# Performance work log

Measured on AMD Instinct MI355X. Metric: run time of the kernel, lower is better.

Reference implementation:

```python
import jax, jax.numpy as jnp
import numpy as np

B, L, D_IN = 16, 2048, 512
HID, H = 512, 8
D = HID // H          # head dim
FACTOR = 5
U = min(FACTOR * int(np.ceil(np.log(L))), L)  # u_q == u_k == 40 (L == S)


def setup_inputs() -> dict:
    key = jax.random.key(0)
    ks = jax.random.split(key, 8)
    s = 1.0 / np.sqrt(D_IN).astype(np.float32)
    return {
        "q_in": jax.random.normal(ks[0], (B, L, D_IN), jnp.float32),
        "k_in": jax.random.normal(ks[1], (B, L, D_IN), jnp.float32),
        "v_in": jax.random.normal(ks[2], (B, L, D_IN), jnp.float32),
        "Wq": jax.random.normal(ks[3], (D_IN, HID), jnp.float32) * s,
        "Wk": jax.random.normal(ks[4], (D_IN, HID), jnp.float32) * s,
        "Wv": jax.random.normal(ks[5], (D_IN, HID), jnp.float32) * s,
        "Wo": jax.random.normal(ks[6], (HID, HID // H), jnp.float32) / np.sqrt(HID).astype(np.float32),
        "indx_q_seq": jax.random.randint(ks[7], (L,), 0, L, dtype=jnp.int32),
    }


def reference(q_in, k_in, v_in, Wq, Wk, Wv, Wo, indx_q_seq):
    # projections + (memory-reinterpreting, as in the TF source) head reshape
    q = (q_in @ Wq).reshape(B, H, L, D)
    k = (k_in @ Wk).reshape(B, H, L, D)
    v = (v_in @ Wv).reshape(B, H, L, D)

    # --- _prob_qk ---
    # TF's chained gathers on the broadcast k_expand collapse to pairing
    # query s with the single key indx_q_seq[s]; all sample_k columns of
    # Q_K_sample are identical, so M = max - sum/L = dot * (1 - U/L).
    k_sel = k[:, :, indx_q_seq, :]                        # [B,H,L,D]
    dot = jnp.einsum('bhle,bhle->bhl', q, k_sel)          # [B,H,L]
    M = dot - dot * (jnp.float32(U) / jnp.float32(L))
    _, m_top = jax.lax.top_k(M, U)                        # [B,H,U]

    b_idx = jnp.arange(B)[:, None, None]
    h_idx = jnp.arange(H)[None, :, None]
    q_red = q[b_idx, h_idx, m_top]                        # [B,H,U,D]
    scores = jnp.einsum('bhue,bhle->bhul', q_red, k)      # [B,H,U,L]
    scores = scores * (1.0 / np.sqrt(D).astype(np.float32))

    # --- initial context: causal cumsum of values ---
    context = jnp.cumsum(v, axis=-2)                      # [B,H,L,D]

    # --- update context at the top-U query positions (causal mask) ---
    causal = jnp.arange(L)[None, None, None, :] > m_top[..., None]
    scores = jnp.where(causal, -jnp.inf, scores)
    attn = jax.nn.softmax(scores, axis=-1)                # [B,H,U,L]
    upd = jnp.einsum('bhul,bhld->bhud', attn, v)          # [B,H,U,D]
    context = context.at[b_idx, h_idx, m_top].set(upd)

    out = context.reshape(B, L, HID) @ Wo                 # [B,L,HID//H]
    return out
```

## Files before the change

### kernel.cpp

```cpp
#include <hip/hip_runtime.h>
#include <hip/hip_bf16.h>
#include <math.h>

#define B_   16
#define L_   2048
#define DIN  512
#define HID_ 512
#define H_   8
#define D_   64
#define U_   40
#define BH   (B_*H_)

typedef unsigned short u16;
typedef unsigned int u32;
typedef unsigned long long u64;
typedef __bf16 bf16x8 __attribute__((ext_vector_type(8)));
typedef float f32x4 __attribute__((ext_vector_type(4)));

__device__ __forceinline__ u16 f2bf(float x) {
  __bf16 b = (__bf16)x;
  return __builtin_bit_cast(unsigned short, b);
}
__device__ __forceinline__ float bf2f(u16 h) {
  return __uint_as_float(((unsigned)h) << 16);
}
__device__ __forceinline__ u32 pk2(float a, float b) {
  return (u32)f2bf(a) | ((u32)f2bf(b) << 16);
}
__device__ __forceinline__ void gload16(const u16* g, u16* l) {
  __builtin_amdgcn_global_load_lds(
      (__attribute__((address_space(1))) void*)(g),
      (__attribute__((address_space(3))) void*)(l), 16, 0, 0);
}
__device__ __forceinline__ void gload16f(const float* g, float* l) {
  __builtin_amdgcn_global_load_lds(
      (__attribute__((address_space(1))) void*)(g),
      (__attribute__((address_space(3))) void*)(l), 16, 0, 0);
}
__device__ __forceinline__ u64 mkkey(float Mv, int l) {
  u32 fb = __float_as_uint(Mv);
  u32 mapped = (fb & 0x80000000u) ? ~fb : (fb | 0x80000000u);
  return ((u64)mapped << 32) | (u64)(0xFFFFFFFFu - (u32)l);
}

__global__ __launch_bounds__(256)
void wsplit3_kernel(const float* __restrict__ Wq, const float* __restrict__ Wk,
                    const float* __restrict__ Wv, u16* __restrict__ Bt3) {
  const float* W = (blockIdx.y == 0) ? Wq : (blockIdx.y == 1) ? Wk : Wv;
  u16* Bt = Bt3 + (size_t)blockIdx.y * 524288;
  int tid = blockIdx.x * 256 + threadIdx.x;
  int n = tid & 511, k = tid >> 9;
  float a = W[(size_t)k * 512 + n];
  u16 hi = f2bf(a);
  u16 lo = f2bf(a - bf2f(hi));
  int kb = k >> 5, kc = k & 31;
  int slotH = kc >> 3, wi = kc & 7;
  int swzH = (slotH     ^ (n & 7)) << 3;
  int swzL = ((4+slotH) ^ (n & 7)) << 3;
  Bt[(size_t)n * 1024 + kb * 64 + swzH + wi] = hi;
  Bt[(size_t)n * 1024 + kb * 64 + swzL + wi] = lo;
}

__global__ __launch_bounds__(256, 2)
void gemm_proj3(const float* __restrict__ A, const u16* __restrict__ Bt,
                float* __restrict__ C) {
  __shared__ float Asf[2][128 * 32];
  __shared__ u16 Bs[2][128 * 64];
  const int bid = blockIdx.x;
  const int g = bid >> 3;
  const int xb = (bid & 7) + ((g >> 2) << 3);
  const int yb = g & 3;
  const int t = threadIdx.x;
  const int w = t >> 6, lane = t & 63;
  const int lhi = lane >> 4, l16 = lane & 15;
  const int row0 = xb * 128, col0 = yb * 128;
  const int wrow = (w >> 1) * 64, wcol = (w & 1) * 64;

  const u16* gB = Bt + (size_t)(col0 + w * 32 + (lane >> 3)) * 1024 + (lane & 7) * 8;
  const int rA0 = w * 32 + (lane >> 3);
  const int swsl = lane & 7;

  f32x4 acc[4][4];
  #pragma unroll
  for (int i = 0; i < 4; ++i)
    #pragma unroll
    for (int j = 0; j < 4; ++j) acc[i][j] = (f32x4){0.f, 0.f, 0.f, 0.f};

#define STAGE3(KB, NB)                                                          \
  { u16* lB = &Bs[NB][(w * 32) * 64];                                           \
    _Pragma("unroll") for (int i = 0; i < 4; ++i)                               \
      gload16(gB + (KB) * 64 + (size_t)i * 8 * 1024, lB + i * 8 * 64);          \
    _Pragma("unroll") for (int i = 0; i < 4; ++i) {                             \
      int r = rA0 + i * 8;                                                      \
      int slot = swsl ^ (r & 7);                                                \
      gload16f(A + (size_t)(row0 + r) * 512 + (KB) * 32 + slot * 4,             \
               &Asf[NB][(w * 32 + i * 8) * 32]); } }

  STAGE3(0, 0)
  asm volatile("s_waitcnt vmcnt(0)" ::: "memory");
  __builtin_amdgcn_s_barrier();

  for (int kb = 0; kb < 16; ++kb) {
    const int cur = kb & 1;
    if (kb < 15) {
      STAGE3(kb + 1, cur ^ 1)
      asm volatile("s_waitcnt vmcnt(8)" ::: "memory");
    } else {
      asm volatile("s_waitcnt vmcnt(0)" ::: "memory");
    }
    __builtin_amdgcn_sched_barrier(0);
    __builtin_amdgcn_s_barrier();

    bf16x8 bfH[4], bfL[4];
    #pragma unroll
    for (int j = 0; j < 4; ++j) {
      int cb = wcol + j * 16 + l16;
      bfH[j] = *reinterpret_cast<const bf16x8*>(
          &Bs[cur][cb * 64 + ((lhi ^ (cb & 7)) << 3)]);
      bfL[j] = *reinterpret_cast<const bf16x8*>(
          &Bs[cur][cb * 64 + (((4 + lhi) ^ (cb & 7)) << 3)]);
    }
    #pragma unroll
    for (int i = 0; i < 4; ++i) {
      int ra = wrow + i * 16 + l16;
      const f32x4 x0 = *reinterpret_cast<const f32x4*>(
          &Asf[cur][ra * 32 + (((lhi * 2)       ^ (ra & 7)) << 2)]);
      const f32x4 x1 = *reinterpret_cast<const f32x4*>(
          &Asf[cur][ra * 32 + ((((lhi * 2) + 1) ^ (ra & 7)) << 2)]);
      bf16x8 aH;
      aH[0] = (__bf16)x0[0]; aH[1] = (__bf16)x0[1];
      aH[2] = (__bf16)x0[2]; aH[3] = (__bf16)x0[3];
      aH[4] = (__bf16)x1[0]; aH[5] = (__bf16)x1[1];
      aH[6] = (__bf16)x1[2]; aH[7] = (__bf16)x1[3];
      #pragma unroll
      for (int j = 0; j < 4; ++j)
        acc[i][j] = __builtin_amdgcn_mfma_f32_16x16x32_bf16(aH, bfH[j], acc[i][j], 0, 0, 0);
      bf16x8 aL;
      aL[0] = (__bf16)(x0[0] - (float)aH[0]); aL[1] = (__bf16)(x0[1] - (float)aH[1]);
      aL[2] = (__bf16)(x0[2] - (float)aH[2]); aL[3] = (__bf16)(x0[3] - (float)aH[3]);
      aL[4] = (__bf16)(x1[0] - (float)aH[4]); aL[5] = (__bf16)(x1[1] - (float)aH[5]);
      aL[6] = (__bf16)(x1[2] - (float)aH[6]); aL[7] = (__bf16)(x1[3] - (float)aH[7]);
      #pragma unroll
      for (int j = 0; j < 4; ++j)
        acc[i][j] = __builtin_amdgcn_mfma_f32_16x16x32_bf16(aH, bfL[j], acc[i][j], 0, 0, 0);
      #pragma unroll
      for (int j = 0; j < 4; ++j)
        acc[i][j] = __builtin_amdgcn_mfma_f32_16x16x32_bf16(aL, bfH[j], acc[i][j], 0, 0, 0);
    }
    __builtin_amdgcn_s_barrier();
    __builtin_amdgcn_sched_barrier(0);
  }
#undef STAGE3
  #pragma unroll
  for (int i = 0; i < 4; ++i)
    #pragma unroll
    for (int j = 0; j < 4; ++j)
      #pragma unroll
      for (int r = 0; r < 4; ++r)
        C[(size_t)(row0 + wrow + i * 16 + lhi * 4 + r) * 512
          + col0 + wcol + j * 16 + l16] = acc[i][j][r];
}

__global__ __launch_bounds__(256, 2)
void gemm_proj_v(const float* __restrict__ A, const u16* __restrict__ Bt,
                 u16* __restrict__ C) {
  __shared__ float Asf[2][128 * 32];
  __shared__ u16 Bs[2][128 * 64];
  const int bid = blockIdx.x;
  const int g = bid >> 3;
  const int xb = (bid & 7) + ((g >> 2) << 3);
  const int yb = g & 3;
  const int t = threadIdx.x;
  const int w = t >> 6, lane = t & 63;
  const int lhi = lane >> 4, l16 = lane & 15;
  const int row0 = xb * 128, col0 = yb * 128;
  const int wrow = (w >> 1) * 64, wcol = (w & 1) * 64;

  const u16* gB = Bt + (size_t)(col0 + w * 32 + (lane >> 3)) * 1024 + (lane & 7) * 8;
  const int rA0 = w * 32 + (lane >> 3);
  const int swsl = lane & 7;

  f32x4 acc[4][4];
  #pragma unroll
  for (int i = 0; i < 4; ++i)
    #pragma unroll
    for (int j = 0; j < 4; ++j) acc[i][j] = (f32x4){0.f, 0.f, 0.f, 0.f};

#define STAGEV(KB, NB)                                                          \
  { u16* lB = &Bs[NB][(w * 32) * 64];                                           \
    _Pragma("unroll") for (int i = 0; i < 4; ++i)                               \
      gload16(gB + (KB) * 64 + (size_t)i * 8 * 1024, lB + i * 8 * 64);          \
    _Pragma("unroll") for (int i = 0; i < 4; ++i) {                             \
      int r = rA0 + i * 8;                                                      \
      int slot = swsl ^ (r & 7);                                                \
      gload16f(A + (size_t)(row0 + r) * 512 + (KB) * 32 + slot * 4,             \
               &Asf[NB][(w * 32 + i * 8) * 32]); } }

  STAGEV(0, 0)
  asm volatile("s_waitcnt vmcnt(0)" ::: "memory");
  __builtin_amdgcn_s_barrier();

  for (int kb = 0; kb < 16; ++kb) {
    const int cur = kb & 1;
    if (kb < 15) {
      STAGEV(kb + 1, cur ^ 1)
      asm volatile("s_waitcnt vmcnt(8)" ::: "memory");
    } else {
      asm volatile("s_waitcnt vmcnt(0)" ::: "memory");
    }
    __builtin_amdgcn_sched_barrier(0);
    __builtin_amdgcn_s_barrier();

    bf16x8 bfH[4];
    #pragma unroll
    for (int j = 0; j < 4; ++j) {
      int cb = wcol + j * 16 + l16;
      bfH[j] = *reinterpret_cast<const bf16x8*>(
          &Bs[cur][cb * 64 + ((lhi ^ (cb & 7)) << 3)]);
    }
    #pragma unroll
    for (int i = 0; i < 4; ++i) {
      int ra = wrow + i * 16 + l16;
      const f32x4 x0 = *reinterpret_cast<const f32x4*>(
          &Asf[cur][ra * 32 + (((lhi * 2)       ^ (ra & 7)) << 2)]);
      const f32x4 x1 = *reinterpret_cast<const f32x4*>(
          &Asf[cur][ra * 32 + ((((lhi * 2) + 1) ^ (ra & 7)) << 2)]);
      bf16x8 aH;
      aH[0] = (__bf16)x0[0]; aH[1] = (__bf16)x0[1];
      aH[2] = (__bf16)x0[2]; aH[3] = (__bf16)x0[3];
      aH[4] = (__bf16)x1[0]; aH[5] = (__bf16)x1[1];
      aH[6] = (__bf16)x1[2]; aH[7] = (__bf16)x1[3];
      #pragma unroll
      for (int j = 0; j < 4; ++j)
        acc[i][j] = __builtin_amdgcn_mfma_f32_16x16x32_bf16(aH, bfH[j], acc[i][j], 0, 0, 0);
    }
    __builtin_amdgcn_s_barrier();
    __builtin_amdgcn_sched_barrier(0);
  }
#undef STAGEV
  #pragma unroll
  for (int i = 0; i < 4; ++i)
    #pragma unroll
    for (int j = 0; j < 4; ++j)
      #pragma unroll
      for (int r = 0; r < 4; ++r)
        C[(size_t)(row0 + wrow + i * 16 + lhi * 4 + r) * 512
          + col0 + wcol + j * 16 + l16] = f2bf(acc[i][j][r]);
}

__global__ __launch_bounds__(256)
void dotsel_kernel(const float* __restrict__ qp, const float* __restrict__ kp,
                   const int* __restrict__ indx, u64* __restrict__ cand) {
  __shared__ u64 keys[256];
  __shared__ u64 wmax[2][4];
  const int bh = blockIdx.x, ch = blockIdx.y;
  const int t = threadIdx.x, w = t >> 6, lane = t & 63;
  const size_t boff = (size_t)bh * 131072;
  const int l0 = ch * 256 + w * 64;
  const float cUL = 40.0f / 2048.0f;
  const int li = lane >> 4;
  const int dq = lane & 15;

  #pragma unroll 8
  for (int i = 0; i < 16; ++i) {
    int l = l0 + i * 4 + li;
    int ls = indx[l];
    float4 q4 = *reinterpret_cast<const float4*>(&qp[boff + (size_t)l * 64 + dq * 4]);
    float4 k4 = *reinterpret_cast<const float4*>(&kp[boff + (size_t)ls * 64 + dq * 4]);
    float p = q4.x * k4.x + q4.y * k4.y + q4.z * k4.z + q4.w * k4.w;
    p += __shfl_xor(p, 1, 64);
    p += __shfl_xor(p, 2, 64);
    p += __shfl_xor(p, 4, 64);
    p += __shfl_xor(p, 8, 64);
    if (dq == 0) {
      float Mv = p - p * cUL;
      keys[w * 64 + i * 4 + li] = mkkey(Mv, l);
    }
  }
  __syncthreads();

  u64 myk = keys[t];
  for (int u = 0; u < U_; ++u) {
    u64 b = myk;
    #pragma unroll
    for (int off = 32; off >= 1; off >>= 1) {
      u64 v = __shfl_xor(b, off, 64);
      if (v > b) b = v;
    }
    if (lane == 0) wmax[u & 1][w] = b;
    __syncthreads();
    const u64* wm = wmax[u & 1];
    u64 m = wm[0];
    if (wm[1] > m) m = wm[1];
    if (wm[2] > m) m = wm[2];
    if (wm[3] > m) m = wm[3];
    if (myk == m) myk = 0;
    if (t == 0) cand[((size_t)(bh * 8 + ch)) * U_ + u] = m;
  }
}

__global__ __launch_bounds__(256)
void merge_topk_wo(const u64* __restrict__ cand, int* __restrict__ mtop,
                   const float* __restrict__ Wo, u16* __restrict__ WoT) {
  const int bh = blockIdx.x;
  const int t = threadIdx.x;
  {
    int tid = bh * 256 + t;
    int j = tid >> 9, k = tid & 511;
    float v = Wo[(size_t)k * 64 + j];
    int k0 = k & ~63, ko = k & 63;
    int ks = ko >> 5, kc = ko & 31;
    int slot = (ks * 4 + (kc >> 3)) ^ (j & 7);
    WoT[(size_t)j * 512 + k0 + (slot << 3) + (kc & 7)] = f2bf(v);
  }
  if (t >= 64) return;
  const int lane = t;
  u64 c0 = cand[(size_t)bh * 320 + 0 * 64 + lane];
  u64 c1 = cand[(size_t)bh * 320 + 1 * 64 + lane];
  u64 c2 = cand[(size_t)bh * 320 + 2 * 64 + lane];
  u64 c3 = cand[(size_t)bh * 320 + 3 * 64 + lane];
  u64 c4 = cand[(size_t)bh * 320 + 4 * 64 + lane];
  for (int u = 0; u < U_; ++u) {
    u64 b = c0;
    if (c1 > b) b = c1;
    if (c2 > b) b = c2;
    if (c3 > b) b = c3;
    if (c4 > b) b = c4;
    #pragma unroll
    for (int off = 32; off >= 1; off >>= 1) {
      u64 v = __shfl_xor(b, off, 64);
      if (v > b) b = v;
    }
    if (c0 == b) c0 = 0;
    if (c1 == b) c1 = 0;
    if (c2 == b) c2 = 0;
    if (c3 == b) c3 = 0;
    if (c4 == b) c4 = 0;
    if (lane == 0) mtop[bh * U_ + u] = (int)(0xFFFFFFFFu - (u32)b);
  }
}

__global__ __launch_bounds__(256)
void gather_q_kernel(const float* __restrict__ qp, const int* __restrict__ mtop,
                     u16* __restrict__ qredbf) {
  int tid = blockIdx.x * 256 + threadIdx.x;
  int s = tid >> 6;
  int d = tid & 63;
  int bh = s / 48;
  int u = s - bh * 48;
  float val = 0.f;
  if (u < U_) {
    int m = mtop[bh * U_ + u];
    val = qp[(size_t)bh * (L_ * D_) + (size_t)m * D_ + d] * 0.125f;
  }
  qredbf[tid] = f2bf(val);
}

__global__ __launch_bounds__(256)
void attn_fused(const u16* __restrict__ qredbf, const float* __restrict__ kp,
                const u16* __restrict__ vbf, const int* __restrict__ mtop,
                float* __restrict__ partial, float* __restrict__ msums) {
  __shared__ u16 As[48 * 64];
  __shared__ u16 Bs[128 * 64];
  __shared__ u16 Ps[48 * 128];
  __shared__ int ms[48];
  __shared__ float redm[4][48];
  __shared__ float reds[4][48];
  const int bh = blockIdx.x, chk = blockIdx.y;
  const int l0 = chk * 128;
  const int t = threadIdx.x, w = t >> 6, lane = t & 63;
  const int lhi = lane >> 4, l16 = lane & 15;

  for (int e = t; e < 384; e += 256) {
    int r = e >> 3, s = e & 7;
    *reinterpret_cast<uint4*>(&As[r * 64 + ((s ^ (r & 7)) << 3)]) =
        *reinterpret_cast<const uint4*>(&qredbf[(size_t)bh * 3072 + e * 8]);
  }
  #pragma unroll
  for (int ee = 0; ee < 4; ++ee) {
    int e = t + ee * 256;
    int r = e >> 3, s = e & 7;
    const float* src = &kp[(size_t)bh * 131072 + (size_t)(l0 + r) * 64 + s * 8];
    float4 va = *reinterpret_cast<const float4*>(src);
    float4 vb = *reinterpret_cast<const float4*>(src + 4);
    uint4 w4 = make_uint4(pk2(va.x, va.y), pk2(va.z, va.w),
                          pk2(vb.x, vb.y), pk2(vb.z, vb.w));
    *reinterpret_cast<uint4*>(&Bs[r * 64 + ((s ^ (r & 7)) << 3)]) = w4;
  }
  if (t < 48) ms[t] = (t < U_) ? mtop[bh * U_ + t] : -1;
  __syncthreads();

  f32x4 acc[3][2];
  #pragma unroll
  for (int m = 0; m < 3; ++m)
    #pragma unroll
    for (int n = 0; n < 2; ++n) acc[m][n] = (f32x4){0.f, 0.f, 0.f, 0.f};
  #pragma unroll
  for (int ks = 0; ks < 2; ++ks) {
    bf16x8 a[3], b[2];
    #pragma unroll
    for (int m = 0; m < 3; ++m) {
      int r = m * 16 + l16;
      a[m] = *reinterpret_cast<const bf16x8*>(
          &As[r * 64 + (((ks * 4 + lhi) ^ (r & 7)) << 3)]);
    }
    #pragma unroll
    for (int n = 0; n < 2; ++n) {
      int cb = w * 32 + n * 16 + l16;
      b[n] = *reinterpret_cast<const bf16x8*>(
          &Bs[cb * 64 + (((ks * 4 + lhi) ^ (cb & 7)) << 3)]);
    }
    #pragma unroll
    for (int m = 0; m < 3; ++m)
      #pragma unroll
      for (int n = 0; n < 2; ++n)
        acc[m][n] = __builtin_amdgcn_mfma_f32_16x16x32_bf16(a[m], b[n], acc[m][n], 0, 0, 0);
  }

  float val[3][2][4], mx[3][4];
  #pragma unroll
  for (int m = 0; m < 3; ++m)
    #pragma unroll
    for (int r = 0; r < 4; ++r) {
      int u = m * 16 + lhi * 4 + r;
      float v0 = acc[m][0][r], v1 = acc[m][1][r];
      if (l0 + w * 32 + 0 * 16 + l16 > ms[u]) v0 = -INFINITY;
      if (l0 + w * 32 + 1 * 16 + l16 > ms[u]) v1 = -INFINITY;
      val[m][0][r] = v0; val[m][1][r] = v1;
      mx[m][r] = fmaxf(v0, v1);
    }
  #pragma unroll
  for (int off = 1; off <= 8; off <<= 1)
    #pragma unroll
    for (int m = 0; m < 3; ++m)
      #pragma unroll
      for (int r = 0; r < 4; ++r)
        mx[m][r] = fmaxf(mx[m][r], __shfl_xor(mx[m][r], off, 64));
  if (l16 == 0) {
    #pragma unroll
    for (int m = 0; m < 3; ++m)
      #pragma unroll
      for (int r = 0; r < 4; ++r)
        redm[w][m * 16 + lhi * 4 + r] = mx[m][r];
  }
  __syncthreads();

  float sx[3][4];
  #pragma unroll
  for (int m = 0; m < 3; ++m)
    #pragma unroll
    for (int r = 0; r < 4; ++r) {
      int u = m * 16 + lhi * 4 + r;
      float mv = fmaxf(fmaxf(redm[0][u], redm[1][u]), fmaxf(redm[2][u], redm[3][u]));
      mv = (mv > -1e30f) ? mv : 0.f;
      float p0 = __expf(val[m][0][r] - mv);
      float p1 = __expf(val[m][1][r] - mv);
      sx[m][r] = p0 + p1;
      {
        int l = w * 32 + 0 * 16 + l16, s = l >> 3;
        int sw = (s & 8) | ((s & 7) ^ (u & 7));
        Ps[u * 128 + (sw << 3) + (l & 7)] = f2bf(p0);
      }
      {
        int l = w * 32 + 1 * 16 + l16, s = l >> 3;
        int sw = (s & 8) | ((s & 7) ^ (u & 7));
        Ps[u * 128 + (sw << 3) + (l & 7)] = f2bf(p1);
      }
    }
  #pragma unroll
  for (int off = 1; off <= 8; off <<= 1)
    #pragma unroll
    for (int m = 0; m < 3; ++m)
      #pragma unroll
      for (int r = 0; r < 4; ++r)
        sx[m][r] += __shfl_xor(sx[m][r], off, 64);
  if (l16 == 0) {
    #pragma unroll
    for (int m = 0; m < 3; ++m)
      #pragma unroll
      for (int r = 0; r < 4; ++r)
        reds[w][m * 16 + lhi * 4 + r] = sx[m][r];
  }
  __syncthreads();

  if (t < 48) {
    float mv = fmaxf(fmaxf(redm[0][t], redm[1][t]), fmaxf(redm[2][t], redm[3][t]));
    mv = (mv > -1e30f) ? mv : 0.f;
    float sv = reds[0][t] + reds[1][t] + reds[2][t] + reds[3][t];
    size_t o = (((size_t)chk * 128 + bh) * 48 + t) * 2;
    msums[o] = mv; msums[o + 1] = sv;
  }
  const size_t vbase = (size_t)bh * 131072;
  #pragma unroll
  for (int j = 0; j < 16; ++j) {
    int ll = w * 32 + 2 * j;
    u16 ua = vbf[vbase + (size_t)(l0 + ll) * 64 + lane];
    u16 ub = vbf[vbase + (size_t)(l0 + ll + 1) * 64 + lane];
    u32 pk = (u32)ua | ((u32)ub << 16);
    int s = ll >> 3;
    int sw = (s & 8) | ((s & 7) ^ (lane & 7));
    *reinterpret_cast<u32*>(&Bs[lane * 128 + (sw << 3) + (ll & 7)]) = pk;
  }
  __syncthreads();

  f32x4 acc2[3];
  #pragma unroll
  for (int m = 0; m < 3; ++m) acc2[m] = (f32x4){0.f, 0.f, 0.f, 0.f};
  #pragma unroll
  for (int ks = 0; ks < 4; ++ks) {
    bf16x8 b;
    { int cb = w * 16 + l16; int s = ks * 4 + lhi;
      int sw = (s & 8) | ((s & 7) ^ (cb & 7));
      b = *reinterpret_cast<const bf16x8*>(&Bs[cb * 128 + (sw << 3)]); }
    #pragma unroll
    for (int m = 0; m < 3; ++m) {
      int r = m * 16 + l16; int s = ks * 4 + lhi;
      int sw = (s & 8) | ((s & 7) ^ (r & 7));
      bf16x8 a = *reinterpret_cast<const bf16x8*>(&Ps[r * 128 + (sw << 3)]);
      acc2[m] = __builtin_amdgcn_mfma_f32_16x16x32_bf16(a, b, acc2[m], 0, 0, 0);
    }
  }
  #pragma unroll
  for (int m = 0; m < 3; ++m)
    #pragma unroll
    for (int r = 0; r < 4; ++r) {
      int u = m * 16 + lhi * 4 + r;
      partial[(((size_t)chk * 128 + bh) * 48 + u) * 64 + w * 16 + l16] = acc2[m][r];
    }
}

__global__ __launch_bounds__(256)
void cumsumA(const u16* __restrict__ vbf, float* __restrict__ seg32) {
  int bh = blockIdx.x, sg = blockIdx.y;
  int t = threadIdx.x, w = t >> 6, lane = t & 63;
  int g = sg * 4 + w;
  size_t base = (size_t)bh * 131072 + (size_t)g * 32 * 64;
  float s = 0.f;
  for (int i = 0; i < 32; ++i) s += bf2f(vbf[base + i * 64 + lane]);
  seg32[((size_t)bh * 64 + g) * 64 + lane] = s;
}
__global__ __launch_bounds__(256)
void cumsumB(const u16* __restrict__ vbf, const float* __restrict__ seg32,
             u16* __restrict__ ctxbf) {
  int bh = blockIdx.x, sg = blockIdx.y;
  int t = threadIdx.x, w = t >> 6, lane = t & 63;
  int g = sg * 4 + w;
  float run = 0.f;
  for (int s = 0; s < g; ++s) run += seg32[((size_t)bh * 64 + s) * 64 + lane];
  size_t base = (size_t)bh * 131072 + (size_t)g * 32 * 64;
  for (int i = 0; i < 32; ++i) {
    run += bf2f(vbf[base + i * 64 + lane]);
    ctxbf[base + i * 64 + lane] = f2bf(run);
  }
}

__global__ __launch_bounds__(256)
void merge_pv_scatter(const float* __restrict__ partial, const float* __restrict__ msums,
                      const int* __restrict__ mtop, u16* __restrict__ ctxbf) {
  int tid = blockIdx.x * 256 + threadIdx.x;
  int s = tid >> 6, d = tid & 63;
  int bh = s / U_, u = s - bh * U_;
  float mg = -INFINITY;
  #pragma unroll
  for (int c = 0; c < 16; ++c)
    mg = fmaxf(mg, msums[(((size_t)c * 128 + bh) * 48 + u) * 2]);
  float av = 0.f, sg = 0.f;
  #pragma unroll
  for (int c = 0; c < 16; ++c) {
    size_t o = (((size_t)c * 128 + bh) * 48 + u) * 2;
    float e = __expf(msums[o] - mg);
    av += partial[(((size_t)c * 128 + bh) * 48 + u) * 64 + d] * e;
    sg += msums[o + 1] * e;
  }
  ctxbf[(size_t)bh * 131072 + (size_t)mtop[s] * 64 + d] = f2bf(av / sg);
}

__global__ __launch_bounds__(256, 6)
void gemm_out(const u16* __restrict__ ctxbf, const u16* __restrict__ WoT,
              float* __restrict__ out) {
  __shared__ u16 As[64 * 64];
  __shared__ u16 Bs[64 * 64];
  const int t = threadIdx.x, w = t >> 6, lane = t & 63;
  const int lhi = lane >> 4, l16 = lane & 15;
  const int row0 = blockIdx.x * 64;
  f32x4 acc[4];
  #pragma unroll
  for (int j = 0; j < 4; ++j) acc[j] = (f32x4){0.f, 0.f, 0.f, 0.f};

  for (int k0 = 0; k0 < 512; k0 += 64) {
    #pragma unroll
    for (int ii = 0; ii < 2; ++ii) {
      int e = t + ii * 256;
      int j = e >> 3, s = e & 7;
      gload16(WoT + (size_t)j * 512 + k0 + s * 8, Bs + (size_t)(w * 64 + ii * 256) * 8);
    }
    #pragma unroll
    for (int ii = 0; ii < 2; ++ii) {
      int e = t + ii * 256;
      int r = e >> 3, s = e & 7;
      gload16(ctxbf + (size_t)(row0 + r) * 512 + k0 + (s ^ (r & 7)) * 8,
              As + (size_t)(w * 64 + ii * 256) * 8);
    }
    __syncthreads();
    #pragma unroll
    for (int ks = 0; ks < 2; ++ks) {
      int r = w * 16 + l16;
      bf16x8 a = *reinterpret_cast<const bf16x8*>(
          &As[r * 64 + (((ks * 4 + lhi) ^ (r & 7)) << 3)]);
      #pragma unroll
      for (int jf = 0; jf < 4; ++jf) {
        int cb = jf * 16 + l16;
        bf16x8 b = *reinterpret_cast<const bf16x8*>(
            &Bs[cb * 64 + (((ks * 4 + lhi) ^ (cb & 7)) << 3)]);
        acc[jf] = __builtin_amdgcn_mfma_f32_16x16x32_bf16(a, b, acc[jf], 0, 0, 0);
      }
    }
    __syncthreads();
  }
  #pragma unroll
  for (int jf = 0; jf < 4; ++jf)
    #pragma unroll
    for (int r = 0; r < 4; ++r)
      out[(size_t)(row0 + w * 16 + lhi * 4 + r) * 64 + jf * 16 + l16] = acc[jf][r];
}

extern "C" void kernel_launch(void* const* d_in, const int* in_sizes, int n_in,
                              void* d_out, int out_size, void* d_ws, size_t ws_size,
                              hipStream_t stream) {
  const float* q_in = (const float*)d_in[0];
  const float* k_in = (const float*)d_in[1];
  const float* v_in = (const float*)d_in[2];
  const float* Wq   = (const float*)d_in[3];
  const float* Wk   = (const float*)d_in[4];
  const float* Wv   = (const float*)d_in[5];
  const float* Wo   = (const float*)d_in[6];
  const int*   indx = (const int*)d_in[7];
  float* out = (float*)d_out;

  float* ws = (float*)d_ws;
  float* qp   = ws;
  float* kp   = ws + 16777216;
  u16*   vbf  = (u16*)(ws + 33554432);
  u64*   cand = (u64*)(ws + 50331648);
  u16*   qredbf = (u16*)(ws + 50593792);
  u16*   WoT  = (u16*)(ws + 50790400);
  int*   mtop = (int*)(ws + 50921472);
  u16*   Bt3  = (u16*)d_out;
  float* partial = qp;
  float* msums   = qp + 6291456;
  u16*   ctxbf = (u16*)kp;
  float* seg32 = kp + 8388608;

  const int M = B_ * L_;

  wsplit3_kernel<<<dim3(1024, 3), 256, 0, stream>>>(Wq, Wk, Wv, Bt3);

  gemm_proj3<<<1024, 256, 0, stream>>>(q_in, Bt3, qp);
  gemm_proj3<<<1024, 256, 0, stream>>>(k_in, Bt3 + 524288, kp);
  gemm_proj_v<<<1024, 256, 0, stream>>>(v_in, Bt3 + 1048576, vbf);

  dotsel_kernel<<<dim3(BH, 8), 256, 0, stream>>>(qp, kp, indx, cand);
  merge_topk_wo<<<BH, 256, 0, stream>>>(cand, mtop, Wo, WoT);
  gather_q_kernel<<<(BH * 48 * 64) / 256, 256, 0, stream>>>(qp, mtop, qredbf);

  attn_fused<<<dim3(BH, 16), 256, 0, stream>>>(qredbf, kp, vbf, mtop, partial, msums);

  cumsumA<<<dim3(BH, 16), 256, 0, stream>>>(vbf, seg32);
  cumsumB<<<dim3(BH, 16), 256, 0, stream>>>(vbf, seg32, ctxbf);
  merge_pv_scatter<<<(BH * U_ * 64) / 256, 256, 0, stream>>>(partial, msums, mtop, ctxbf);

  gemm_out<<<M / 64, 256, 0, stream>>>(ctxbf, WoT, out);
}
```

Baseline: 323.2 us.

## Drop double buffering in Q/K projection GEMM to raise occupancy

Replaces the two-stage LDS double-buffered pipeline in the Q/K projection GEMM with a single buffer, loading each k-block and then synchronizing before compute. This halves shared memory per block and raises the launch-bounds occupancy hint from 2 to 4 blocks per CU, relying on more resident waves to hide global-load latency instead of explicit prefetch. The trade-off is that load/compute overlap inside a block disappears and each iteration needs two full barriers. Register pressure must also fit the tighter bound or spills may occur.

```diff
diff --git a/kernel.cpp b/kernel.cpp
--- a/kernel.cpp
+++ b/kernel.cpp
@@ -61,11 +61,11 @@
   Bt[(size_t)n * 1024 + kb * 64 + swzL + wi] = lo;
 }
 
-__global__ __launch_bounds__(256, 2)
+__global__ __launch_bounds__(256, 4)
 void gemm_proj3(const float* __restrict__ A, const u16* __restrict__ Bt,
                 float* __restrict__ C) {
-  __shared__ float Asf[2][128 * 32];
-  __shared__ u16 Bs[2][128 * 64];
+  __shared__ float Asf[128 * 32];
+  __shared__ u16 Bs[128 * 64];
   const int bid = blockIdx.x;
   const int g = bid >> 3;
   const int xb = (bid & 7) + ((g >> 2) << 3);
@@ -77,6 +77,7 @@
   const int wrow = (w >> 1) * 64, wcol = (w & 1) * 64;
 
   const u16* gB = Bt + (size_t)(col0 + w * 32 + (lane >> 3)) * 1024 + (lane & 7) * 8;
+  u16* lB = &Bs[(w * 32) * 64];
   const int rA0 = w * 32 + (lane >> 3);
   const int swsl = lane & 7;
 
@@ -86,47 +87,35 @@
     #pragma unroll
     for (int j = 0; j < 4; ++j) acc[i][j] = (f32x4){0.f, 0.f, 0.f, 0.f};
 
-#define STAGE3(KB, NB)                                                          \
-  { u16* lB = &Bs[NB][(w * 32) * 64];                                           \
-    _Pragma("unroll") for (int i = 0; i < 4; ++i)                               \
-      gload16(gB + (KB) * 64 + (size_t)i * 8 * 1024, lB + i * 8 * 64);          \
-    _Pragma("unroll") for (int i = 0; i < 4; ++i) {                             \
-      int r = rA0 + i * 8;                                                      \
-      int slot = swsl ^ (r & 7);                                                \
-      gload16f(A + (size_t)(row0 + r) * 512 + (KB) * 32 + slot * 4,             \
-               &Asf[NB][(w * 32 + i * 8) * 32]); } }
-
-  STAGE3(0, 0)
-  asm volatile("s_waitcnt vmcnt(0)" ::: "memory");
-  __builtin_amdgcn_s_barrier();
-
   for (int kb = 0; kb < 16; ++kb) {
-    const int cur = kb & 1;
-    if (kb < 15) {
-      STAGE3(kb + 1, cur ^ 1)
-      asm volatile("s_waitcnt vmcnt(8)" ::: "memory");
-    } else {
-      asm volatile("s_waitcnt vmcnt(0)" ::: "memory");
-    }
-    __builtin_amdgcn_sched_barrier(0);
-    __builtin_amdgcn_s_barrier();
+    #pragma unroll
+    for (int i = 0; i < 4; ++i)
+      gload16(gB + kb * 64 + (size_t)i * 8 * 1024, lB + i * 8 * 64);
+    #pragma unroll
+    for (int i = 0; i < 4; ++i) {
+      int r = rA0 + i * 8;
+      int slot = swsl ^ (r & 7);
+      gload16f(A + (size_t)(row0 + r) * 512 + kb * 32 + slot * 4,
+               &Asf[(w * 32 + i * 8) * 32]);
+    }
+    __syncthreads();
 
     bf16x8 bfH[4], bfL[4];
     #pragma unroll
     for (int j = 0; j < 4; ++j) {
       int cb = wcol + j * 16 + l16;
       bfH[j] = *reinterpret_cast<const bf16x8*>(
-          &Bs[cur][cb * 64 + ((lhi ^ (cb & 7)) << 3)]);
+          &Bs[cb * 64 + ((lhi ^ (cb & 7)) << 3)]);
       bfL[j] = *reinterpret_cast<const bf16x8*>(
-          &Bs[cur][cb * 64 + (((4 + lhi) ^ (cb & 7)) << 3)]);
+          &Bs[cb * 64 + (((4 + lhi) ^ (cb & 7)) << 3)]);
     }
     #pragma unroll
     for (int i = 0; i < 4; ++i) {
       int ra = wrow + i * 16 + l16;
       const f32x4 x0 = *reinterpret_cast<const f32x4*>(
-          &Asf[cur][ra * 32 + (((lhi * 2)       ^ (ra & 7)) << 2)]);
+          &Asf[ra * 32 + (((lhi * 2)       ^ (ra & 7)) << 2)]);
       const f32x4 x1 = *reinterpret_cast<const f32x4*>(
-          &Asf[cur][ra * 32 + ((((lhi * 2) + 1) ^ (ra & 7)) << 2)]);
+          &Asf[ra * 32 + ((((lhi * 2) + 1) ^ (ra & 7)) << 2)]);
       bf16x8 aH;
       aH[0] = (__bf16)x0[0]; aH[1] = (__bf16)x0[1];
       aH[2] = (__bf16)x0[2]; aH[3] = (__bf16)x0[3];
@@ -147,10 +136,8 @@
       for (int j = 0; j < 4; ++j)
         acc[i][j] = __builtin_amdgcn_mfma_f32_16x16x32_bf16(aL, bfH[j], acc[i][j], 0, 0, 0);
     }
-    __builtin_amdgcn_s_barrier();
-    __builtin_amdgcn_sched_barrier(0);
-  }
-#undef STAGE3
+    __syncthreads();
+  }
   #pragma unroll
   for (int i = 0; i < 4; ++i)
     #pragma unroll
```

Result: no change. 324.9 us (+0.5%).
